# Performance work log

Hardware: AMD Instinct MI355X
Metric: run time of the kernel (lower is better)

Reference implementation:

```python
import jax, jax.numpy as jnp
import numpy as np

NUM_HEADS = 16
WINDOW = 256  # window_size: each query i attends to keys [max(0, i-W+1), i]


def setup_inputs() -> dict:
    key = jax.random.key(0)
    k1, k2, k3, k4, k5 = jax.random.split(key, 5)
    B, S, D = 2, 4096, 1024
    scale = 0.02
    return {
        "x": jax.random.normal(k1, (B, S, D), dtype=jnp.float32),
        "wq": jax.random.normal(k2, (D, D), dtype=jnp.float32) * scale,
        "wk": jax.random.normal(k3, (D, D), dtype=jnp.float32) * scale,
        "wv": jax.random.normal(k4, (D, D), dtype=jnp.float32) * scale,
        "wo": jax.random.normal(k5, (D, D), dtype=jnp.float32) * scale,
    }


def _sliding_window_attn(x, wq, wk, wv, wo):
    B, S, D = x.shape
    H, W = NUM_HEADS, WINDOW
    Dh = D // H
    nb = S // W  # number of query blocks (S assumed divisible by W)

    def proj(w):
        # nn.Linear: y = x @ w.T ; -> [B, H, nb, W, Dh]
        y = (x @ w.T).reshape(B, nb, W, H, Dh)
        return y.transpose(0, 3, 1, 2, 4)

    q = proj(wq)
    k = proj(wk)
    v = proj(wv)

    # Each query block j attends to key blocks j-1 and j (banded causal window).
    zpad = jnp.zeros((B, H, 1, W, Dh), dtype=x.dtype)
    kpad = jnp.concatenate([zpad, k], axis=2)  # [B,H,nb+1,W,Dh]
    vpad = jnp.concatenate([zpad, v], axis=2)
    k2 = jnp.concatenate([kpad[:, :, :-1], kpad[:, :, 1:]], axis=3)  # [B,H,nb,2W,Dh]
    v2 = jnp.concatenate([vpad[:, :, :-1], vpad[:, :, 1:]], axis=3)

    scores = jnp.einsum("bhjqd,bhjkd->bhjqk", q, k2) / jnp.sqrt(
        jnp.asarray(Dh, dtype=x.dtype)
    )  # [B,H,nb,W,2W]

    # Mask: query global pos i = j*W + qi; key global pos kp = (j-1)*W + ki.
    # Valid iff i-W+1 <= kp <= i  <=>  qi+1 <= ki <= qi+W ; and kp >= 0.
    qi = jnp.arange(W)[:, None]          # [W,1]
    ki = jnp.arange(2 * W)[None, :]      # [1,2W]
    band = (ki >= qi + 1) & (ki <= qi + W)                      # [W,2W]
    kpos_ok = (jnp.arange(nb)[:, None, None] - 1) * W + ki[None] >= 0  # [nb,1,2W]
    mask = band[None] & kpos_ok          # [nb,W,2W]

    neg = jnp.finfo(scores.dtype).min
    scores = jnp.where(mask[None, None], scores, neg)
    attn = jax.nn.softmax(scores, axis=-1)

    out = jnp.einsum("bhjqk,bhjkd->bhjqd", attn, v2)  # [B,H,nb,W,Dh]
    out = out.transpose(0, 2, 3, 1, 4).reshape(B, S, D)
    return out @ wo.T


def reference(x, wq, wk, wv, wo):
    return _sliding_window_attn(x, wq, wk, wv, wo)
```

## Files before the change

kernel.cpp:

```cpp
#include <hip/hip_runtime.h>

#define S_LEN 4096
#define DMODEL 1024
#define NH 16
#define DH 64
#define WIN 256
#define NQKV 3072

typedef __attribute__((ext_vector_type(8))) short short8;
typedef __attribute__((ext_vector_type(4))) short sh4;
typedef __attribute__((ext_vector_type(4))) float floatx4;

__device__ __forceinline__ ushort f2bf(float f) {
    union { float f; unsigned int i; } x;
    x.f = f;
    unsigned int r = x.i + 0x7FFFu + ((x.i >> 16) & 1u);
    return (ushort)(r >> 16);
}

__global__ __launch_bounds__(256) void cvt_all(const float* __restrict__ x,
                                               const float* __restrict__ wq,
                                               const float* __restrict__ wk,
                                               const float* __restrict__ wv,
                                               const float* __restrict__ wo,
                                               ushort* __restrict__ xb,
                                               ushort* __restrict__ W3b,
                                               ushort* __restrict__ wob,
                                               int nx8, int nw8) {
    int i = blockIdx.x * 256 + threadIdx.x;
    const float* src;
    ushort* dst;
    if (i < nx8) {
        src = x + (size_t)i * 8;            dst = xb + (size_t)i * 8;
    } else {
        int j = i - nx8;
        int which = j / nw8, r = j - which * nw8;
        if (which >= 4) return;
        const float* w4[4] = {wq, wk, wv, wo};
        src = w4[which] + (size_t)r * 8;
        dst = (which == 3 ? wob : W3b + (size_t)which * nw8 * 8) + (size_t)r * 8;
    }
    floatx4 f0 = *(const floatx4*)src;
    floatx4 f1 = *(const floatx4*)(src + 4);
    short8 v;
#pragma unroll
    for (int e = 0; e < 4; ++e) v[e] = (short)f2bf(f0[e]);
#pragma unroll
    for (int e = 0; e < 4; ++e) v[4 + e] = (short)f2bf(f1[e]);
    *(short8*)dst = v;
}

#define GLOAD16(src, dst)                                                     \
    __builtin_amdgcn_global_load_lds(                                         \
        (const __attribute__((address_space(1))) void*)(src),                 \
        (__attribute__((address_space(3))) void*)(dst), 16, 0, 0)

template <bool OUTF32>
__global__ __launch_bounds__(256, 2) void gemm128(const ushort* __restrict__ A,
                                                  const ushort* __restrict__ W,
                                                  void* __restrict__ Cout,
                                                  int M, int N, int K) {
    __shared__ __align__(16) ushort As[128 * 64];
    __shared__ __align__(16) ushort Ws[256 * 64];

    const int tid = threadIdx.x;
    const int w = tid >> 6, l = tid & 63;

    int bx, by;
    {
        const int nbx = gridDim.x, nby = gridDim.y;
        if ((nby & 7) == 0) {
            const int lin = blockIdx.y * nbx + blockIdx.x;
            const int rpb = nby >> 3;
            const int xcd = lin & 7, idx = lin >> 3;
            bx = idx / rpb;
            by = xcd * rpb + (idx - bx * rpb);
        } else {
            bx = blockIdx.x;
            by = blockIdx.y;
        }
    }
    const int bm0 = by * 128, bn0 = bx * 256;
    const int wm = (w >> 1) * 64, wn = (w & 1) * 128;
    const int lm = l & 15, quad = l >> 4;

    floatx4 acc[4][8] = {};

    int arow[4], acol[4];
#pragma unroll
    for (int p = 0; p < 4; ++p) {
        int c = p * 256 + tid;
        arow[p] = c >> 3;
        acol[p] = (((c & 7) ^ (arow[p] & 7))) * 8;
    }
    int wrow[8], wcol[8];
#pragma unroll
    for (int p = 0; p < 8; ++p) {
        int c = p * 256 + tid;
        wrow[p] = c >> 3;
        wcol[p] = (((c & 7) ^ (wrow[p] & 7))) * 8;
    }

    for (int k0 = 0; k0 < K; k0 += 64) {
#pragma unroll
        for (int p = 0; p < 4; ++p)
            GLOAD16(A + (size_t)(bm0 + arow[p]) * K + k0 + acol[p],
                    As + p * 2048 + tid * 8);
#pragma unroll
        for (int p = 0; p < 8; ++p)
            GLOAD16(W + (size_t)(bn0 + wrow[p]) * K + k0 + wcol[p],
                    Ws + p * 2048 + tid * 8);
        __syncthreads();

#pragma unroll
        for (int kk = 0; kk < 2; ++kk) {
            const int sseg = ((kk * 4 + quad) ^ (lm & 7)) * 8;
            short8 af[4], wf[8];
#pragma unroll
            for (int mi = 0; mi < 4; ++mi)
                af[mi] = *(const short8*)&As[(wm + mi * 16 + lm) * 64 + sseg];
#pragma unroll
            for (int ni = 0; ni < 8; ++ni)
                wf[ni] = *(const short8*)&Ws[(wn + ni * 16 + lm) * 64 + sseg];
#pragma unroll
            for (int mi = 0; mi < 4; ++mi)
#pragma unroll
                for (int ni = 0; ni < 8; ++ni)
                    acc[mi][ni] = __builtin_amdgcn_mfma_f32_16x16x32_bf16(
                        af[mi], wf[ni], acc[mi][ni], 0, 0, 0);
        }
        __syncthreads();
    }

#pragma unroll
    for (int mi = 0; mi < 4; ++mi)
#pragma unroll
        for (int ni = 0; ni < 8; ++ni)
#pragma unroll
            for (int r = 0; r < 4; ++r) {
                int row = bm0 + wm + mi * 16 + quad * 4 + r;
                int col = bn0 + wn + ni * 16 + lm;
                if constexpr (OUTF32)
                    ((float*)Cout)[(size_t)row * N + col] = acc[mi][ni][r];
                else
                    ((ushort*)Cout)[(size_t)row * N + col] = f2bf(acc[mi][ni][r]);
            }
}

#define VTP 136
#define PSP 40

__global__ __launch_bounds__(256) void swattn_mfma(const ushort* __restrict__ QKV,
                                                   ushort* __restrict__ O) {
    __shared__ __align__(16) ushort Vt[64 * VTP];
    __shared__ __align__(16) ushort Ps[2][4 * 64 * PSP];
    __shared__ __align__(16) float lW[256];

    const int j = blockIdx.x, h = blockIdx.y, b = blockIdx.z;
    const int tid = threadIdx.x;
    const int w = tid >> 6, l = tid & 63;
    const int quad = l >> 4, lc = l & 15;

    const size_t base = (size_t)b * S_LEN * NQKV + (size_t)h * DH;
    const ushort* Qp = QKV + base;
    const ushort* Kp = QKV + base + DMODEL;
    const ushort* Vp = QKV + base + 2 * DMODEL;

    short8 qf[4][2];
#pragma unroll
    for (int nq = 0; nq < 4; ++nq)
#pragma unroll
        for (int kk = 0; kk < 2; ++kk)
            qf[nq][kk] = *(const short8*)(Qp +
                (size_t)(j * 256 + w * 64 + nq * 16 + lc) * NQKV + kk * 32 + quad * 8);

    floatx4 o[4][4] = {};
    float lsum[4] = {0.f, 0.f, 0.f, 0.f};

    const float sscale = 0.18033688011112042f;
    const float M0 = 2.0f;
    const int qlo = w * 64, qhi = w * 64 + 63;

    for (int c = 0; c < 4; ++c) {
        const int kg0 = (j - 1) * 256 + c * 128;
        if (kg0 < 0) continue;
        __syncthreads();
#pragma unroll
        for (int i = 0; i < 4; ++i) {
            int cc = i * 256 + tid, key = cc >> 3, seg = cc & 7;
            short8 vv = *(const short8*)(Vp + (size_t)(kg0 + key) * NQKV + seg * 8);
#pragma unroll
            for (int e = 0; e < 8; ++e)
                Vt[(e * 8 + seg) * VTP + key] = (ushort)vv[e];
        }
        __syncthreads();

        const int krel0 = c * 128 - 256;
#pragma unroll
        for (int g = 0; g < 4; ++g) {
            const int k0 = krel0 + g * 32;
            if (k0 > qhi || k0 + 31 < qlo - 255) continue;
            ushort* Pw = &Ps[g & 1][w * 64 * PSP];

            floatx4 st[2][4];
            const floatx4 zero = {};
#pragma unroll
            for (int kt = 0; kt < 2; ++kt) {
                const ushort* Kr = Kp + (size_t)(kg0 + g * 32 + kt * 16 + lc) * NQKV;
                short8 kf0 = *(const short8*)(Kr + quad * 8);
                short8 kf1 = *(const short8*)(Kr + 32 + quad * 8);
#pragma unroll
                for (int nq = 0; nq < 4; ++nq) {
                    int kmin = k0 + kt * 16, qmin = qlo + nq * 16;
                    if (kmin > qmin + 15 || kmin + 270 < qmin) {
                        st[kt][nq] = zero;
                        continue;
                    }
                    st[kt][nq] = __builtin_amdgcn_mfma_f32_16x16x32_bf16(kf0, qf[nq][0], zero, 0, 0, 0);
                    st[kt][nq] = __builtin_amdgcn_mfma_f32_16x16x32_bf16(kf1, qf[nq][1], st[kt][nq], 0, 0, 0);
                }
            }
#pragma unroll
            for (int kt = 0; kt < 2; ++kt)
#pragma unroll
                for (int nq = 0; nq < 4; ++nq) {
                    sh4 pv;
                    int kmin = k0 + kt * 16, qmin = qlo + nq * 16;
                    if (kmin > qmin + 15 || kmin + 270 < qmin) {
                        pv[0] = pv[1] = pv[2] = pv[3] = 0;
                    } else if (kmin + 15 <= qmin && kmin + 240 >= qmin) {
#pragma unroll
                        for (int r = 0; r < 4; ++r) {
                            float p = exp2f(st[kt][nq][r] * sscale - M0);
                            lsum[nq] += p;
                            pv[r] = (short)f2bf(p);
                        }
                    } else {
#pragma unroll
                        for (int r = 0; r < 4; ++r) {
                            int krel = kmin + quad * 4 + r;
                            int qrel = qmin + lc;
                            bool valid = (krel <= qrel) && (krel + 255 >= qrel);
                            float p = valid ? exp2f(st[kt][nq][r] * sscale - M0) : 0.f;
                            lsum[nq] += p;
                            pv[r] = (short)f2bf(p);
                        }
                    }
                    *(sh4*)&Pw[(nq * 16 + lc) * PSP + kt * 16 + quad * 4] = pv;
                }
            __threadfence_block();

            short8 vf[4];
#pragma unroll
            for (int nd = 0; nd < 4; ++nd) {
                int prow = (lc & 7) * 8 + nd * 2 + (lc >> 3);
                vf[nd] = *(const short8*)&Vt[prow * VTP + g * 32 + quad * 8];
            }
#pragma unroll
            for (int mq = 0; mq < 4; ++mq) {
                int qmin = qlo + mq * 16;
                if (k0 > qmin + 15 || k0 + 286 < qmin) continue;
                short8 pf = *(const short8*)&Pw[(mq * 16 + lc) * PSP + quad * 8];
#pragma unroll
                for (int nd = 0; nd < 4; ++nd)
                    o[mq][nd] = __builtin_amdgcn_mfma_f32_16x16x32_bf16(pf, vf[nd], o[mq][nd], 0, 0, 0);
            }
        }
    }

#pragma unroll
    for (int nq = 0; nq < 4; ++nq) {
        lsum[nq] += __shfl_xor(lsum[nq], 16);
        lsum[nq] += __shfl_xor(lsum[nq], 32);
    }
    if (l < 16) {
#pragma unroll
        for (int nq = 0; nq < 4; ++nq) lW[w * 64 + nq * 16 + l] = lsum[nq];
    }
    __threadfence_block();
#pragma unroll
    for (int mq = 0; mq < 4; ++mq) {
        floatx4 lv = *(const floatx4*)&lW[w * 64 + mq * 16 + quad * 4];
#pragma unroll
        for (int r = 0; r < 4; ++r) {
            float inv = 1.f / lv[r];
            int token = j * 256 + w * 64 + mq * 16 + quad * 4 + r;
#pragma unroll
            for (int nd = 0; nd < 4; ++nd)
                O[(size_t)b * S_LEN * DMODEL + (size_t)token * DMODEL + h * DH + nd * 16 + lc] =
                    f2bf(o[mq][nd][r] * inv);
        }
    }
}

extern "C" void kernel_launch(void* const* d_in, const int* in_sizes, int n_in,
                              void* d_out, int out_size, void* d_ws, size_t ws_size,
                              hipStream_t stream) {
    const float* x  = (const float*)d_in[0];
    const float* wq = (const float*)d_in[1];
    const float* wk = (const float*)d_in[2];
    const float* wv = (const float*)d_in[3];
    const float* wo = (const float*)d_in[4];
    float* out = (float*)d_out;

    const int D = DMODEL;
    const int M = in_sizes[0] / D;
    const int Bb = M / S_LEN;

    ushort* xb   = (ushort*)d_ws;
    ushort* W3b  = xb + (size_t)M * D;
    ushort* wob  = W3b + (size_t)NQKV * D;
    ushort* QKVb = wob + (size_t)D * D;
    ushort* Ob   = xb;

    const int nx8 = M * D / 8, nw8 = D * D / 8;
    const int ntot = nx8 + 4 * nw8;
    cvt_all<<<dim3((ntot + 255) / 256), dim3(256), 0, stream>>>(
        x, wq, wk, wv, wo, xb, W3b, wob, nx8, nw8);

    gemm128<false><<<dim3(NQKV / 256, M / 128), dim3(256), 0, stream>>>(
        xb, W3b, QKVb, M, NQKV, D);

    swattn_mfma<<<dim3(S_LEN / WIN, NH, Bb), dim3(256), 0, stream>>>(QKVb, Ob);

    gemm128<true><<<dim3(D / 256, M / 128), dim3(256), 0, stream>>>(
        Ob, wob, out, M, D, D);
}
```

Measured before the change: 229.7 us.

## Stage K tiles in shared memory and register-prefetch next K/V chunk

K chunks are now loaded cooperatively into a padded shared-memory tile instead of each wave reading K fragments straight from global memory. The next chunk's K and V are prefetched into registers while the current chunk is being computed, overlapping global loads with MFMA work. This costs extra LDS (about 18 KB more) and 32 more VGPRs per thread for the prefetch buffers, which may lower occupancy.

```diff
diff --git a/kernel.cpp b/kernel.cpp
--- a/kernel.cpp
+++ b/kernel.cpp
@@ -147,11 +147,13 @@
             }
 }
 
+#define KSP 72
 #define VTP 136
 #define PSP 40
 
 __global__ __launch_bounds__(256) void swattn_mfma(const ushort* __restrict__ QKV,
                                                    ushort* __restrict__ O) {
+    __shared__ __align__(16) ushort Ks[128 * KSP];
     __shared__ __align__(16) ushort Vt[64 * VTP];
     __shared__ __align__(16) ushort Ps[2][4 * 64 * PSP];
     __shared__ __align__(16) float lW[256];
@@ -181,19 +183,44 @@
     const float M0 = 2.0f;
     const int qlo = w * 64, qhi = w * 64 + 63;
 
-    for (int c = 0; c < 4; ++c) {
-        const int kg0 = (j - 1) * 256 + c * 128;
-        if (kg0 < 0) continue;
+    int skey[4], sseg[4];
+#pragma unroll
+    for (int i = 0; i < 4; ++i) {
+        int cc = i * 256 + tid;
+        skey[i] = cc >> 3;
+        sseg[i] = cc & 7;
+    }
+
+    short8 kreg[4], vreg[4];
+    const int c0 = (j == 0) ? 2 : 0;
+    {
+        const int kg0 = (j - 1) * 256 + c0 * 128;
+#pragma unroll
+        for (int i = 0; i < 4; ++i) {
+            kreg[i] = *(const short8*)(Kp + (size_t)(kg0 + skey[i]) * NQKV + sseg[i] * 8);
+            vreg[i] = *(const short8*)(Vp + (size_t)(kg0 + skey[i]) * NQKV + sseg[i] * 8);
+        }
+    }
+
+    for (int c = c0; c < 4; ++c) {
         __syncthreads();
 #pragma unroll
         for (int i = 0; i < 4; ++i) {
-            int cc = i * 256 + tid, key = cc >> 3, seg = cc & 7;
-            short8 vv = *(const short8*)(Vp + (size_t)(kg0 + key) * NQKV + seg * 8);
+            *(short8*)&Ks[skey[i] * KSP + sseg[i] * 8] = kreg[i];
 #pragma unroll
             for (int e = 0; e < 8; ++e)
-                Vt[(e * 8 + seg) * VTP + key] = (ushort)vv[e];
+                Vt[(e * 8 + sseg[i]) * VTP + skey[i]] = (ushort)vreg[i][e];
         }
         __syncthreads();
+
+        if (c < 3) {
+            const int kg0n = (j - 1) * 256 + (c + 1) * 128;
+#pragma unroll
+            for (int i = 0; i < 4; ++i) {
+                kreg[i] = *(const short8*)(Kp + (size_t)(kg0n + skey[i]) * NQKV + sseg[i] * 8);
+                vreg[i] = *(const short8*)(Vp + (size_t)(kg0n + skey[i]) * NQKV + sseg[i] * 8);
+            }
+        }
 
         const int krel0 = c * 128 - 256;
 #pragma unroll
@@ -206,9 +233,8 @@
             const floatx4 zero = {};
 #pragma unroll
             for (int kt = 0; kt < 2; ++kt) {
-                const ushort* Kr = Kp + (size_t)(kg0 + g * 32 + kt * 16 + lc) * NQKV;
-                short8 kf0 = *(const short8*)(Kr + quad * 8);
-                short8 kf1 = *(const short8*)(Kr + 32 + quad * 8);
+                short8 kf0 = *(const short8*)&Ks[(g * 32 + kt * 16 + lc) * KSP + quad * 8];
+                short8 kf1 = *(const short8*)&Ks[(g * 32 + kt * 16 + lc) * KSP + 32 + quad * 8];
 #pragma unroll
                 for (int nq = 0; nq < 4; ++nq) {
                     int kmin = k0 + kt * 16, qmin = qlo + nq * 16;
```

Measured after the change: 226.1 us. About the same (-1.6%).
